# Performance work log

Measured on AMD Instinct MI355X. Metric: run time of the kernel, lower is better.

The kernel has to match this reference:

```python
import jax, jax.numpy as jnp
import numpy as np

BLOCK = 32       # MX block size
EMAX_E4M3 = 8.0  # max exponent of fp8 e4m3 (max normal = 448 = 1.75 * 2^8)
NUM_HEADS = 16


def _e4m3_round(v):
    """Round values to fp8 e4m3 grid (bias 7, 3 mantissa bits, subnormals, max 448)."""
    absv = jnp.abs(v)
    e = jnp.floor(jnp.log2(jnp.where(absv > 0, absv, 1.0)))
    e = jnp.maximum(e, -6.0)                # min normal exponent; below -> subnormal grid
    step = jnp.exp2(e - 3.0)                # 3 mantissa bits
    q = jnp.round(v / step) * step          # round-half-even like IEEE
    q = jnp.clip(q, -448.0, 448.0)
    return jnp.where(absv > 0, q, jnp.zeros_like(q))


def _mx_quantize(x):
    """Blockwise (32 along last dim) shared-exponent (E8M0) fp8 e4m3 quant-dequant."""
    shp = x.shape
    xb = x.reshape(shp[:-1] + (shp[-1] // BLOCK, BLOCK))
    amax = jnp.max(jnp.abs(xb), axis=-1, keepdims=True)
    sexp = jnp.floor(jnp.log2(jnp.where(amax > 0, amax, 1.0))) - EMAX_E4M3
    sexp = jnp.clip(sexp, -127.0, 127.0)    # E8M0 scale range
    scale = jnp.where(amax > 0, jnp.exp2(sexp), jnp.ones_like(sexp))
    q = _e4m3_round(xb / scale) * scale
    return q.reshape(shp)


def mxq(x):
    return _mx_quantize(x)


def _mx_linear(x, W, b):
    # quantize activations and weights (blocks of 32 along the contraction dim)
    return jnp.einsum('bse,oe->bso', mxq(x), mxq(W)) + b


def setup_inputs() -> dict:
    key = jax.random.key(0)
    ks = jax.random.split(key, 9)
    B, S, E = 4, 1024, 1024
    inp = {
        'query': jax.random.normal(ks[0], (B, S, E), dtype=jnp.float32),
        'Wq': jax.random.normal(ks[1], (E, E), dtype=jnp.float32) * 0.02,
        'bq': jnp.zeros((E,), dtype=jnp.float32),
        'Wk': jax.random.normal(ks[2], (E, E), dtype=jnp.float32) * 0.02,
        'bk': jnp.zeros((E,), dtype=jnp.float32),
        'Wv': jax.random.normal(ks[3], (E, E), dtype=jnp.float32) * 0.02,
        'bv': jnp.zeros((E,), dtype=jnp.float32),
        'Wo': jax.random.normal(ks[4], (E, E), dtype=jnp.float32) * 0.02,
        'bo': jnp.zeros((E,), dtype=jnp.float32),
    }
    return inp


def reference(query, Wq, bq, Wk, bk, Wv, bv, Wo, bo):
    B, S, E = query.shape
    H = NUM_HEADS
    D = E // H
    Q = _mx_linear(query, Wq, bq).reshape(B, S, H, D).transpose(0, 2, 1, 3)
    K = _mx_linear(query, Wk, bk).reshape(B, S, H, D).transpose(0, 2, 1, 3)
    V = _mx_linear(query, Wv, bv).reshape(B, S, H, D).transpose(0, 2, 1, 3)
    scores = jnp.einsum('bhqd,bhkd->bhqk', Q, K) / jnp.sqrt(jnp.float32(D))
    scores = mxq(scores)                    # score quantizer (blocks of 32 along kv dim)
    attn = jax.nn.softmax(scores, axis=-1)  # dropout p=0 -> identity
    ctx = jnp.einsum('bhqk,bhkd->bhqd', attn, V)
    ctx = ctx.transpose(0, 2, 1, 3).reshape(B, S, E)
    return _mx_linear(ctx, Wo, bo)
```

## Files before the change

kernel.cpp:

```cpp
#include <hip/hip_runtime.h>
#include <hip/hip_bf16.h>
#include <cstdint>
#include <cstddef>


#define S_LEN 1024
#define E_DIM 1024
#define NH    16
#define DH    64
#define BATCH 4
#define NROWS (BATCH * S_LEN)

typedef short          bf16x8  __attribute__((ext_vector_type(8)));
typedef float          f32x4   __attribute__((ext_vector_type(4)));
typedef unsigned short u16x8   __attribute__((ext_vector_type(8)));
typedef unsigned short u16x4   __attribute__((ext_vector_type(4)));
typedef unsigned int   u32x4   __attribute__((ext_vector_type(4)));


__device__ __forceinline__ void mx_scale_bits(float amax, float& scale, float& inv) {
  int eb = (int)(__float_as_uint(amax) >> 23);
  int sb = eb - 8;
  sb = sb < 1 ? 1 : (sb > 253 ? 253 : sb);
  float sc = __uint_as_float((unsigned)sb << 23);
  float iv = __uint_as_float((unsigned)(254 - sb) << 23);
  bool nz = (amax > 0.0f);
  scale = nz ? sc : 1.0f;
  inv   = nz ? iv : 1.0f;
}

__device__ __forceinline__ void qdq2(float& a, float& b) {
  a = fminf(fmaxf(a, -448.0f), 448.0f);
  b = fminf(fmaxf(b, -448.0f), 448.0f);
  int p = __builtin_amdgcn_cvt_pk_fp8_f32(a, b, 0, false);
  a = __builtin_amdgcn_cvt_f32_fp8(p, 0);
  b = __builtin_amdgcn_cvt_f32_fp8(p, 1);
}

__device__ __forceinline__ unsigned short f32_to_bf16_rne(float f) {
  unsigned u = __float_as_uint(f);
  unsigned r = 0x7FFFu + ((u >> 16) & 1u);
  return (unsigned short)((u + r) >> 16);
}

__device__ __forceinline__ float quad_red_max(float x) {
  auto p = __builtin_amdgcn_permlane16_swap(__float_as_uint(x), __float_as_uint(x), false, false);
  x = fmaxf(__uint_as_float(p[0]), __uint_as_float(p[1]));
  auto q = __builtin_amdgcn_permlane32_swap(__float_as_uint(x), __float_as_uint(x), false, false);
  return fmaxf(__uint_as_float(q[0]), __uint_as_float(q[1]));
}
__device__ __forceinline__ float quad_red_min(float x) {
  auto p = __builtin_amdgcn_permlane16_swap(__float_as_uint(x), __float_as_uint(x), false, false);
  x = fminf(__uint_as_float(p[0]), __uint_as_float(p[1]));
  auto q = __builtin_amdgcn_permlane32_swap(__float_as_uint(x), __float_as_uint(x), false, false);
  return fminf(__uint_as_float(q[0]), __uint_as_float(q[1]));
}
__device__ __forceinline__ float quad_red_sum(float x) {
  auto p = __builtin_amdgcn_permlane16_swap(__float_as_uint(x), __float_as_uint(x), false, false);
  x = __uint_as_float(p[0]) + __uint_as_float(p[1]);
  auto q = __builtin_amdgcn_permlane32_swap(__float_as_uint(x), __float_as_uint(x), false, false);
  return __uint_as_float(q[0]) + __uint_as_float(q[1]);
}


__device__ __forceinline__ void mxq_body(const float* __restrict__ in,
                                         unsigned short* __restrict__ out, int b) {
  const float4* p = (const float4*)(in + (size_t)b * 32);
  float v[32];
#pragma unroll
  for (int g = 0; g < 8; ++g) {
    float4 t = p[g];
    v[g * 4 + 0] = t.x; v[g * 4 + 1] = t.y; v[g * 4 + 2] = t.z; v[g * 4 + 3] = t.w;
  }
  float amax = 0.0f;
#pragma unroll
  for (int i = 0; i < 32; ++i) amax = fmaxf(amax, __builtin_fabsf(v[i]));
  float scale, inv;
  mx_scale_bits(amax, scale, inv);
  u16x8* q = (u16x8*)(out + (size_t)b * 32);
#pragma unroll
  for (int g = 0; g < 4; ++g) {
    u16x8 o;
#pragma unroll
    for (int e = 0; e < 8; e += 2) {
      float a = v[g * 8 + e] * inv, c = v[g * 8 + e + 1] * inv;
      qdq2(a, c);
      o[e]     = (unsigned short)(__float_as_uint(a * scale) >> 16);
      o[e + 1] = (unsigned short)(__float_as_uint(c * scale) >> 16);
    }
    q[g] = o;
  }
}

__global__ __launch_bounds__(256)
void mxq_all(const float* __restrict__ x,
             const float* __restrict__ w0, const float* __restrict__ w1,
             const float* __restrict__ w2, const float* __restrict__ w3,
             unsigned short* __restrict__ ox,
             unsigned short* __restrict__ o0, unsigned short* __restrict__ o1,
             unsigned short* __restrict__ o2, unsigned short* __restrict__ o3) {
  int blk = blockIdx.x;
  const float* in;
  unsigned short* out;
  int base;
  if (blk < 512)      { in = x;  out = ox; base = blk; }
  else if (blk < 640) { in = w0; out = o0; base = blk - 512; }
  else if (blk < 768) { in = w1; out = o1; base = blk - 640; }
  else if (blk < 896) { in = w2; out = o2; base = blk - 768; }
  else                { in = w3; out = o3; base = blk - 896; }
  mxq_body(in, out, base * 256 + threadIdx.x);
}


__global__ __launch_bounds__(256)
void gemm_qkv(const unsigned short* __restrict__ XQ,
              const unsigned short* __restrict__ Wqw, const unsigned short* __restrict__ Wkw,
              const unsigned short* __restrict__ Wvw,
              const float* __restrict__ bq, const float* __restrict__ bk,
              const float* __restrict__ bv,
              unsigned short* __restrict__ Qhi, unsigned short* __restrict__ Qlo,
              unsigned short* __restrict__ Khi, unsigned short* __restrict__ Klo,
              unsigned short* __restrict__ Vthi, unsigned short* __restrict__ Vtlo) {
  const int z = blockIdx.z;
  const unsigned short* Bw = (z == 0) ? Wqw : (z == 1) ? Wkw : Wvw;
  const float* bias = (z == 0) ? bq : (z == 1) ? bk : bv;
  unsigned short* Phi = (z == 0) ? Qhi : (z == 1) ? Khi : Vthi;
  unsigned short* Plo = (z == 0) ? Qlo : (z == 1) ? Klo : Vtlo;
  const float pre = (z == 0) ? 0.125f : 1.0f;

  __shared__ unsigned short sA[128 * 64];
  __shared__ unsigned short sB[128 * 64];
  const int tid = threadIdx.x;
  const int w = tid >> 6, ln = tid & 63;
  const int bm = blockIdx.y * 128, bn = blockIdx.x * 128;
  const int wm = (w >> 1) * 64, wn = (w & 1) * 64;
  const int quad = ln >> 4, col = ln & 15;

  f32x4 acc[4][4];
  f32x4 zero = {0.0f, 0.0f, 0.0f, 0.0f};
#pragma unroll
  for (int i = 0; i < 4; ++i)
#pragma unroll
    for (int j = 0; j < 4; ++j) acc[i][j] = zero;

  const int srow = ln >> 3;
  const int gsw  = (ln & 7) ^ srow;
  const int xo0 = (quad ^ (ln & 7)) * 8;
  const int xo1 = ((quad ^ 4) ^ (ln & 7)) * 8;

  for (int k0 = 0; k0 < 1024; k0 += 64) {
    __syncthreads();
#pragma unroll
    for (int q = 0; q < 4; ++q) {
      int row = w * 32 + q * 8 + srow;
      const unsigned short* ga = XQ + (size_t)(bm + row) * 1024 + k0 + gsw * 8;
      const unsigned short* gb = Bw + (size_t)(bn + row) * 1024 + k0 + gsw * 8;
      __builtin_amdgcn_global_load_lds(
          (const __attribute__((address_space(1))) unsigned int*)ga,
          (__attribute__((address_space(3))) unsigned int*)(sA + (w * 32 + q * 8) * 64),
          16, 0, 0);
      __builtin_amdgcn_global_load_lds(
          (const __attribute__((address_space(1))) unsigned int*)gb,
          (__attribute__((address_space(3))) unsigned int*)(sB + (w * 32 + q * 8) * 64),
          16, 0, 0);
    }
    __syncthreads();

#pragma unroll
    for (int ks = 0; ks < 2; ++ks) {
      const int xo = ks ? xo1 : xo0;
      bf16x8 af[4], bf[4];
#pragma unroll
      for (int t = 0; t < 4; ++t) {
        af[t] = *(const bf16x8*)(sA + (wm + t * 16 + col) * 64 + xo);
        bf[t] = *(const bf16x8*)(sB + (wn + t * 16 + col) * 64 + xo);
      }
#pragma unroll
      for (int ti = 0; ti < 4; ++ti)
#pragma unroll
        for (int tj = 0; tj < 4; ++tj)
          acc[ti][tj] = __builtin_amdgcn_mfma_f32_16x16x32_bf16(af[ti], bf[tj], acc[ti][tj], 0, 0, 0);
    }
  }

#pragma unroll
  for (int ti = 0; ti < 4; ++ti) {
#pragma unroll
    for (int tj = 0; tj < 4; ++tj) {
      int n = bn + wn + tj * 16 + col;
      float bv_ = bias[n];
      if (z != 2) {
#pragma unroll
        for (int i = 0; i < 4; ++i) {
          int m = bm + wm + ti * 16 + quad * 4 + i;
          float v = (acc[ti][tj][i] + bv_) * pre;
          unsigned short h = f32_to_bf16_rne(v);
          float hf = __uint_as_float((unsigned)h << 16);
          Phi[(size_t)m * 1024 + n] = h;
          Plo[(size_t)m * 1024 + n] = f32_to_bf16_rne(v - hf);
        }
      } else {
        int m0 = bm + wm + ti * 16 + quad * 4;
        u16x4 h4, l4;
#pragma unroll
        for (int i = 0; i < 4; ++i) {
          float v = acc[ti][tj][i] + bv_;
          unsigned short h = f32_to_bf16_rne(v);
          float hf = __uint_as_float((unsigned)h << 16);
          h4[i] = h;
          l4[i] = f32_to_bf16_rne(v - hf);
        }
        size_t idx = ((size_t)((m0 >> 10) * 1024 + n)) * 1024 + (m0 & 1023);
        *(u16x4*)(Phi + idx) = h4;
        *(u16x4*)(Plo + idx) = l4;
      }
    }
  }
}


__global__ __launch_bounds__(256)
void gemm_o(const unsigned short* __restrict__ A, const unsigned short* __restrict__ Bw,
            const float* __restrict__ bias, float* __restrict__ C) {
  __shared__ unsigned short sA[64 * 64];
  __shared__ unsigned short sB[128 * 64];
  const int tid = threadIdx.x;
  const int w = tid >> 6, ln = tid & 63;
  const int bm = blockIdx.y * 64, bn = blockIdx.x * 128;
  const int wr = (w >> 1) * 32, wc = (w & 1) * 64;
  const int quad = ln >> 4, col = ln & 15;

  f32x4 acc[2][4];
  f32x4 zero = {0.0f, 0.0f, 0.0f, 0.0f};
#pragma unroll
  for (int i = 0; i < 2; ++i)
#pragma unroll
    for (int j = 0; j < 4; ++j) acc[i][j] = zero;

  const int srow = ln >> 3;
  const int gsw  = (ln & 7) ^ srow;
  const int xo0 = (quad ^ (ln & 7)) * 8;
  const int xo1 = ((quad ^ 4) ^ (ln & 7)) * 8;

  for (int k0 = 0; k0 < 1024; k0 += 64) {
    __syncthreads();
#pragma unroll
    for (int qa = 0; qa < 2; ++qa) {
      int row = w * 16 + qa * 8 + srow;
      __builtin_amdgcn_global_load_lds(
          (const __attribute__((address_space(1))) unsigned int*)(A + (size_t)(bm + row) * 1024 + k0 + gsw * 8),
          (__attribute__((address_space(3))) unsigned int*)(sA + (w * 16 + qa * 8) * 64),
          16, 0, 0);
    }
#pragma unroll
    for (int qb = 0; qb < 4; ++qb) {
      int row = w * 32 + qb * 8 + srow;
      __builtin_amdgcn_global_load_lds(
          (const __attribute__((address_space(1))) unsigned int*)(Bw + (size_t)(bn + row) * 1024 + k0 + gsw * 8),
          (__attribute__((address_space(3))) unsigned int*)(sB + (w * 32 + qb * 8) * 64),
          16, 0, 0);
    }
    __syncthreads();

#pragma unroll
    for (int ks = 0; ks < 2; ++ks) {
      const int xo = ks ? xo1 : xo0;
      bf16x8 af[2], bf[4];
#pragma unroll
      for (int t = 0; t < 2; ++t)
        af[t] = *(const bf16x8*)(sA + (wr + t * 16 + col) * 64 + xo);
#pragma unroll
      for (int t = 0; t < 4; ++t)
        bf[t] = *(const bf16x8*)(sB + (wc + t * 16 + col) * 64 + xo);
#pragma unroll
      for (int ti = 0; ti < 2; ++ti)
#pragma unroll
        for (int tj = 0; tj < 4; ++tj)
          acc[ti][tj] = __builtin_amdgcn_mfma_f32_16x16x32_bf16(af[ti], bf[tj], acc[ti][tj], 0, 0, 0);
    }
  }

#pragma unroll
  for (int ti = 0; ti < 2; ++ti) {
#pragma unroll
    for (int tj = 0; tj < 4; ++tj) {
      int n = bn + wc + tj * 16 + col;
      float bv_ = bias[n];
#pragma unroll
      for (int i = 0; i < 4; ++i) {
        int m = bm + wr + ti * 16 + quad * 4 + i;
        C[(size_t)m * 1024 + n] = acc[ti][tj][i] + bv_;
      }
    }
  }
}


__global__ __launch_bounds__(256, 4)
void attn_kernel(const unsigned short* __restrict__ Qhi, const unsigned short* __restrict__ Qlo,
                 const unsigned short* __restrict__ Khi, const unsigned short* __restrict__ Klo,
                 const unsigned short* __restrict__ Vthi, const unsigned short* __restrict__ Vtlo,
                 unsigned short* __restrict__ ctxq) {
  const int tid = threadIdx.x;
  const int id = blockIdx.y * 16 + blockIdx.x;
  const int qt = (id >> 3) & 15;
  const int bh = ((id >> 7) << 3) | (id & 7);
  const int b = bh >> 4, h = bh & 15;
  const int w = tid >> 6, ln = tid & 63, quad = ln >> 4, col = ln & 15;

  __shared__ __align__(16) short sK[16384];

  bf16x8 qh[2], ql[2];
  {
    const size_t qoff = (size_t)(b * 1024 + qt * 64 + w * 16 + col) * 1024 + h * 64 + quad * 8;
    qh[0] = *(const bf16x8*)(Qhi + qoff);
    qh[1] = *(const bf16x8*)(Qhi + qoff + 32);
    ql[0] = *(const bf16x8*)(Qlo + qoff);
    ql[1] = *(const bf16x8*)(Qlo + qoff + 32);
  }

  const unsigned short* gplane = (w == 0) ? Khi : (w == 1) ? Klo : (w == 2) ? Vthi : Vtlo;
  short* splane = sK + w * 4096;
  const int r8 = ln >> 3;
  const int ch = (ln & 7) ^ r8;
  const unsigned short* bp = (w < 2)
      ? gplane + (size_t)(b * 1024 + r8) * 1024 + h * 64 + ch * 8
      : gplane + (size_t)(b * 1024 + h * 64 + r8) * 1024 + ch * 8;
  const int ktstep = (w < 2) ? 65536 : 64;

  const int xo0 = (quad ^ (col & 7)) * 8;
  const int xo1 = ((quad + 4) ^ (col & 7)) * 8;

  f32x4 o[4];
  f32x4 zero = {0.0f, 0.0f, 0.0f, 0.0f};
#pragma unroll
  for (int t = 0; t < 4; ++t) o[t] = zero;
  float m_ = -3.0e38f, l_ = 0.0f;

  const float LOG2E = 1.44269504088896340736f;

#pragma unroll 1
  for (int kt = 0; kt < 16; ++kt) {
    __syncthreads();
#pragma unroll
    for (int g = 0; g < 8; ++g) {
      __builtin_amdgcn_global_load_lds(
          (const __attribute__((address_space(1))) unsigned int*)(bp + g * 8192),
          (__attribute__((address_space(3))) unsigned int*)(splane + g * 512),
          16, 0, 0);
    }
    bp += ktstep;
    __syncthreads();

    f32x4 s[4];
#pragma unroll
    for (int t = 0; t < 4; ++t) s[t] = zero;
#pragma unroll
    for (int t = 0; t < 4; ++t) {
      const int rb = (t * 16 + col) * 64;
#pragma unroll
      for (int ks = 0; ks < 2; ++ks) {
        const int xo = ks ? xo1 : xo0;
        bf16x8 kh = *(const bf16x8*)(sK +        rb + xo);
        bf16x8 kl = *(const bf16x8*)(sK + 4096 + rb + xo);
        s[t] = __builtin_amdgcn_mfma_f32_16x16x32_bf16(kh, ql[ks], s[t], 0, 0, 0);
        s[t] = __builtin_amdgcn_mfma_f32_16x16x32_bf16(kl, qh[ks], s[t], 0, 0, 0);
        s[t] = __builtin_amdgcn_mfma_f32_16x16x32_bf16(kh, qh[ks], s[t], 0, 0, 0);
      }
    }

    float mx0 = fmaxf(fmaxf(fmaxf(s[0][0], s[0][1]), fmaxf(s[0][2], s[0][3])),
                      fmaxf(fmaxf(s[1][0], s[1][1]), fmaxf(s[1][2], s[1][3])));
    float mn0 = fminf(fminf(fminf(s[0][0], s[0][1]), fminf(s[0][2], s[0][3])),
                      fminf(fminf(s[1][0], s[1][1]), fminf(s[1][2], s[1][3])));
    float mx1 = fmaxf(fmaxf(fmaxf(s[2][0], s[2][1]), fmaxf(s[2][2], s[2][3])),
                      fmaxf(fmaxf(s[3][0], s[3][1]), fmaxf(s[3][2], s[3][3])));
    float mn1 = fminf(fminf(fminf(s[2][0], s[2][1]), fminf(s[2][2], s[2][3])),
                      fminf(fminf(s[3][0], s[3][1]), fminf(s[3][2], s[3][3])));
    mx0 = quad_red_max(mx0); mn0 = quad_red_min(mn0);
    mx1 = quad_red_max(mx1); mn1 = quad_red_min(mn1);

    float sc0, iv0, sc1, iv1;
    mx_scale_bits(fmaxf(mx0, -mn0), sc0, iv0);
    mx_scale_bits(fmaxf(mx1, -mn1), sc1, iv1);
    float scl0 = sc0 * LOG2E, scl1 = sc1 * LOG2E;
#pragma unroll
    for (int t = 0; t < 4; ++t) {
      float iv  = (t < 2) ? iv0 : iv1;
      float scl = (t < 2) ? scl0 : scl1;
      float q0 = s[t][0] * iv, q1 = s[t][1] * iv;
      qdq2(q0, q1);
      float q2 = s[t][2] * iv, q3 = s[t][3] * iv;
      qdq2(q2, q3);
      s[t][0] = q0 * scl; s[t][1] = q1 * scl;
      s[t][2] = q2 * scl; s[t][3] = q3 * scl;
    }
    float d0 = mx0 * iv0, d1 = mx1 * iv1;
    qdq2(d0, d1);
    float mt = fmaxf(d0 * scl0, d1 * scl1);

    float mnew  = fmaxf(m_, mt);
    float alpha = __builtin_amdgcn_exp2f(m_ - mnew);
    m_ = mnew;
    l_ *= alpha;
#pragma unroll
    for (int t = 0; t < 4; ++t) {
      float p0 = __builtin_amdgcn_exp2f(s[t][0] - mnew);
      float p1 = __builtin_amdgcn_exp2f(s[t][1] - mnew);
      float p2 = __builtin_amdgcn_exp2f(s[t][2] - mnew);
      float p3 = __builtin_amdgcn_exp2f(s[t][3] - mnew);
      s[t][0] = p0; s[t][1] = p1; s[t][2] = p2; s[t][3] = p3;
      l_ += (p0 + p1) + (p2 + p3);
    }
#pragma unroll
    for (int nt = 0; nt < 4; ++nt)
#pragma unroll
      for (int i = 0; i < 4; ++i) o[nt][i] *= alpha;

    unsigned Wh[4][2], Wl[4][2];
#pragma unroll
    for (int t = 0; t < 4; ++t) {
#pragma unroll
      for (int u = 0; u < 2; ++u) {
        float a = s[t][2 * u], c = s[t][2 * u + 1];
        __hip_bfloat162 h2 = __float22bfloat162_rn(make_float2(a, c));
        unsigned uh = *(unsigned*)&h2;
        float af = __uint_as_float(uh << 16);
        float cf = __uint_as_float(uh & 0xffff0000u);
        __hip_bfloat162 l2 = __float22bfloat162_rn(make_float2(a - af, c - cf));
        Wh[t][u] = uh;
        Wl[t][u] = *(unsigned*)&l2;
      }
    }
    bf16x8 pah[2], pal[2];
#pragma unroll
    for (int ks = 0; ks < 2; ++ks) {
      auto a0  = __builtin_amdgcn_permlane32_swap(Wh[2 * ks][0], Wh[2 * ks + 1][0], false, false);
      auto j02 = __builtin_amdgcn_permlane16_swap(a0[0], a0[1], false, false);
      auto a1  = __builtin_amdgcn_permlane32_swap(Wh[2 * ks][1], Wh[2 * ks + 1][1], false, false);
      auto j13 = __builtin_amdgcn_permlane16_swap(a1[0], a1[1], false, false);
      u32x4 hw; hw[0] = j02[0]; hw[1] = j13[0]; hw[2] = j02[1]; hw[3] = j13[1];
      pah[ks] = __builtin_bit_cast(bf16x8, hw);
      auto b0  = __builtin_amdgcn_permlane32_swap(Wl[2 * ks][0], Wl[2 * ks + 1][0], false, false);
      auto k02 = __builtin_amdgcn_permlane16_swap(b0[0], b0[1], false, false);
      auto b1  = __builtin_amdgcn_permlane32_swap(Wl[2 * ks][1], Wl[2 * ks + 1][1], false, false);
      auto k13 = __builtin_amdgcn_permlane16_swap(b1[0], b1[1], false, false);
      u32x4 lw; lw[0] = k02[0]; lw[1] = k13[0]; lw[2] = k02[1]; lw[3] = k13[1];
      pal[ks] = __builtin_bit_cast(bf16x8, lw);
    }

#pragma unroll
    for (int nt = 0; nt < 4; ++nt) {
      const int rb = (nt * 16 + col) * 64;
#pragma unroll
      for (int ks = 0; ks < 2; ++ks) {
        const int xo = ks ? xo1 : xo0;
        bf16x8 vh = *(const bf16x8*)(sK +  8192 + rb + xo);
        bf16x8 vl = *(const bf16x8*)(sK + 12288 + rb + xo);
        o[nt] = __builtin_amdgcn_mfma_f32_16x16x32_bf16(vh, pal[ks], o[nt], 0, 0, 0);
        o[nt] = __builtin_amdgcn_mfma_f32_16x16x32_bf16(vl, pah[ks], o[nt], 0, 0, 0);
        o[nt] = __builtin_amdgcn_mfma_f32_16x16x32_bf16(vh, pah[ks], o[nt], 0, 0, 0);
      }
    }
  }

  float linv = 1.0f / quad_red_sum(l_);
#pragma unroll
  for (int nt = 0; nt < 4; ++nt)
#pragma unroll
    for (int i = 0; i < 4; ++i) o[nt][i] *= linv;

  float am0 = 0.0f, am1 = 0.0f;
#pragma unroll
  for (int i = 0; i < 4; ++i) {
    am0 = fmaxf(am0, fmaxf(__builtin_fabsf(o[0][i]), __builtin_fabsf(o[1][i])));
    am1 = fmaxf(am1, fmaxf(__builtin_fabsf(o[2][i]), __builtin_fabsf(o[3][i])));
  }
  am0 = quad_red_max(am0);
  am1 = quad_red_max(am1);
  float sc0, iv0, sc1, iv1;
  mx_scale_bits(am0, sc0, iv0);
  mx_scale_bits(am1, sc1, iv1);

  const int tok = b * 1024 + qt * 64 + w * 16 + col;
  const size_t base = (size_t)tok * 1024 + h * 64 + quad * 4;
#pragma unroll
  for (int nt = 0; nt < 4; ++nt) {
    float iv = (nt < 2) ? iv0 : iv1;
    float sc = (nt < 2) ? sc0 : sc1;
    float q0 = o[nt][0] * iv, q1 = o[nt][1] * iv;
    qdq2(q0, q1);
    float q2 = o[nt][2] * iv, q3 = o[nt][3] * iv;
    qdq2(q2, q3);
    u16x4 h4;
    h4[0] = (unsigned short)(__float_as_uint(q0 * sc) >> 16);
    h4[1] = (unsigned short)(__float_as_uint(q1 * sc) >> 16);
    h4[2] = (unsigned short)(__float_as_uint(q2 * sc) >> 16);
    h4[3] = (unsigned short)(__float_as_uint(q3 * sc) >> 16);
    *(u16x4*)(ctxq + base + nt * 16) = h4;
  }
}


extern "C" void kernel_launch(void* const* d_in, const int* in_sizes, int n_in,
                              void* d_out, int out_size, void* d_ws, size_t ws_size,
                              hipStream_t stream) {
  (void)in_sizes; (void)n_in; (void)out_size; (void)ws_size;
  const float* x  = (const float*)d_in[0];
  const float* Wq = (const float*)d_in[1];
  const float* bq = (const float*)d_in[2];
  const float* Wk = (const float*)d_in[3];
  const float* bk = (const float*)d_in[4];
  const float* Wv = (const float*)d_in[5];
  const float* bv = (const float*)d_in[6];
  const float* Wo = (const float*)d_in[7];
  const float* bo = (const float*)d_in[8];

  char* wsb = (char*)d_ws;
  const size_t MB = (size_t)1 << 20;
  unsigned short* XQb   = (unsigned short*)(wsb + 0);
  unsigned short* WQb   = (unsigned short*)(wsb + 8 * MB);
  unsigned short* WKb   = (unsigned short*)(wsb + 10 * MB);
  unsigned short* WVb   = (unsigned short*)(wsb + 12 * MB);
  unsigned short* WOb   = (unsigned short*)(wsb + 14 * MB);
  unsigned short* Qhi   = (unsigned short*)(wsb + 16 * MB);
  unsigned short* Qlo   = (unsigned short*)(wsb + 24 * MB);
  unsigned short* Khi   = (unsigned short*)(wsb + 32 * MB);
  unsigned short* Klo   = (unsigned short*)(wsb + 40 * MB);
  unsigned short* Vthi  = (unsigned short*)(wsb + 48 * MB);
  unsigned short* Vtlo  = (unsigned short*)(wsb + 56 * MB);
  unsigned short* CTXQb = XQb;

  mxq_all<<<1024, 256, 0, stream>>>(x, Wq, Wk, Wv, Wo, XQb, WQb, WKb, WVb, WOb);

  dim3 qkvgrid(E_DIM / 128, NROWS / 128, 3);
  gemm_qkv<<<qkvgrid, 256, 0, stream>>>(XQb, WQb, WKb, WVb, bq, bk, bv,
                                        Qhi, Qlo, Khi, Klo, Vthi, Vtlo);

  dim3 agrid(16, 64);
  attn_kernel<<<agrid, 256, 0, stream>>>(Qhi, Qlo, Khi, Klo, Vthi, Vtlo, CTXQb);

  dim3 ogrid(E_DIM / 128, NROWS / 64);
  gemm_o<<<ogrid, 256, 0, stream>>>(CTXQb, WOb, bo, (float*)d_out);
}
```

Measured before the change: 234.6 us.

## Double-buffer projection GEMMs, remap blocks per XCD, and skip softmax rescaling

Both projection GEMMs now use double-buffered LDS: the next K tile is prefetched with global_load_lds while the current one feeds the MFMAs, with explicit vmcnt waits and barriers replacing the two syncthreads per iteration. Block indices are remapped so consecutive blocks on the same XCD share M rows, which is meant to improve L2 reuse. The attention kernel now skips the online-softmax max update and the rescaling of the accumulator unless some lane's tile max exceeds the running max by more than 4 (log2 units). The extra LDS halves the number of resident blocks, and the lazy rescale lets exponentials reach up to 2^4 before renormalising.

```diff
diff --git a/kernel.cpp b/kernel.cpp
--- a/kernel.cpp
+++ b/kernel.cpp
@@ -128,11 +128,13 @@
   unsigned short* Plo = (z == 0) ? Qlo : (z == 1) ? Klo : Vtlo;
   const float pre = (z == 0) ? 0.125f : 1.0f;
 
-  __shared__ unsigned short sA[128 * 64];
-  __shared__ unsigned short sB[128 * 64];
+  __shared__ unsigned short sA[2][128 * 64];
+  __shared__ unsigned short sB[2][128 * 64];
   const int tid = threadIdx.x;
   const int w = tid >> 6, ln = tid & 63;
-  const int bm = blockIdx.y * 128, bn = blockIdx.x * 128;
+  const int fid = blockIdx.y * 8 + blockIdx.x;
+  const int xcd = fid & 7, sq = fid >> 3;
+  const int bm = (xcd * 4 + (sq & 3)) * 128, bn = (sq >> 2) * 128;
   const int wm = (w >> 1) * 64, wn = (w & 1) * 64;
   const int quad = ln >> 4, col = ln & 15;
 
@@ -148,8 +150,7 @@
   const int xo0 = (quad ^ (ln & 7)) * 8;
   const int xo1 = ((quad ^ 4) ^ (ln & 7)) * 8;
 
-  for (int k0 = 0; k0 < 1024; k0 += 64) {
-    __syncthreads();
+  auto STAGE = [&](int bb, int k0) {
 #pragma unroll
     for (int q = 0; q < 4; ++q) {
       int row = w * 32 + q * 8 + srow;
@@ -157,30 +158,47 @@
       const unsigned short* gb = Bw + (size_t)(bn + row) * 1024 + k0 + gsw * 8;
       __builtin_amdgcn_global_load_lds(
           (const __attribute__((address_space(1))) unsigned int*)ga,
-          (__attribute__((address_space(3))) unsigned int*)(sA + (w * 32 + q * 8) * 64),
+          (__attribute__((address_space(3))) unsigned int*)(&sA[bb][0] + (w * 32 + q * 8) * 64),
           16, 0, 0);
       __builtin_amdgcn_global_load_lds(
           (const __attribute__((address_space(1))) unsigned int*)gb,
-          (__attribute__((address_space(3))) unsigned int*)(sB + (w * 32 + q * 8) * 64),
+          (__attribute__((address_space(3))) unsigned int*)(&sB[bb][0] + (w * 32 + q * 8) * 64),
           16, 0, 0);
     }
-    __syncthreads();
-
+  };
+
+  STAGE(0, 0);
+#pragma unroll 1
+  for (int k0 = 0; k0 < 1024; k0 += 64) {
+    const int cur = (k0 >> 6) & 1;
+    if (k0 < 960) {
+      STAGE(cur ^ 1, k0 + 64);
+      asm volatile("s_waitcnt vmcnt(8)" ::: "memory");
+    } else {
+      asm volatile("s_waitcnt vmcnt(0)" ::: "memory");
+    }
+    __builtin_amdgcn_s_barrier();
+    __builtin_amdgcn_sched_barrier(0);
+
+    const unsigned short* pA = &sA[cur][0];
+    const unsigned short* pB = &sB[cur][0];
 #pragma unroll
     for (int ks = 0; ks < 2; ++ks) {
       const int xo = ks ? xo1 : xo0;
-      bf16x8 af[4], bf[4];
+      bf16x8 af[4], bfr[4];
 #pragma unroll
       for (int t = 0; t < 4; ++t) {
-        af[t] = *(const bf16x8*)(sA + (wm + t * 16 + col) * 64 + xo);
-        bf[t] = *(const bf16x8*)(sB + (wn + t * 16 + col) * 64 + xo);
+        af[t]  = *(const bf16x8*)(pA + (wm + t * 16 + col) * 64 + xo);
+        bfr[t] = *(const bf16x8*)(pB + (wn + t * 16 + col) * 64 + xo);
       }
 #pragma unroll
       for (int ti = 0; ti < 4; ++ti)
 #pragma unroll
         for (int tj = 0; tj < 4; ++tj)
-          acc[ti][tj] = __builtin_amdgcn_mfma_f32_16x16x32_bf16(af[ti], bf[tj], acc[ti][tj], 0, 0, 0);
-    }
+          acc[ti][tj] = __builtin_amdgcn_mfma_f32_16x16x32_bf16(af[ti], bfr[tj], acc[ti][tj], 0, 0, 0);
+    }
+    __builtin_amdgcn_sched_barrier(0);
+    __builtin_amdgcn_s_barrier();
   }
 
 #pragma unroll
@@ -222,11 +240,13 @@
 __global__ __launch_bounds__(256)
 void gemm_o(const unsigned short* __restrict__ A, const unsigned short* __restrict__ Bw,
             const float* __restrict__ bias, float* __restrict__ C) {
-  __shared__ unsigned short sA[64 * 64];
-  __shared__ unsigned short sB[128 * 64];
+  __shared__ unsigned short sA[2][64 * 64];
+  __shared__ unsigned short sB[2][128 * 64];
   const int tid = threadIdx.x;
   const int w = tid >> 6, ln = tid & 63;
-  const int bm = blockIdx.y * 64, bn = blockIdx.x * 128;
+  const int fid = blockIdx.y * 8 + blockIdx.x;
+  const int xcd = fid & 7, sq = fid >> 3;
+  const int bm = (xcd * 8 + (sq & 7)) * 64, bn = (sq >> 3) * 128;
   const int wr = (w >> 1) * 32, wc = (w & 1) * 64;
   const int quad = ln >> 4, col = ln & 15;
 
@@ -242,14 +262,13 @@
   const int xo0 = (quad ^ (ln & 7)) * 8;
   const int xo1 = ((quad ^ 4) ^ (ln & 7)) * 8;
 
-  for (int k0 = 0; k0 < 1024; k0 += 64) {
-    __syncthreads();
+  auto STAGE = [&](int bb, int k0) {
 #pragma unroll
     for (int qa = 0; qa < 2; ++qa) {
       int row = w * 16 + qa * 8 + srow;
       __builtin_amdgcn_global_load_lds(
           (const __attribute__((address_space(1))) unsigned int*)(A + (size_t)(bm + row) * 1024 + k0 + gsw * 8),
-          (__attribute__((address_space(3))) unsigned int*)(sA + (w * 16 + qa * 8) * 64),
+          (__attribute__((address_space(3))) unsigned int*)(&sA[bb][0] + (w * 16 + qa * 8) * 64),
           16, 0, 0);
     }
 #pragma unroll
@@ -257,27 +276,44 @@
       int row = w * 32 + qb * 8 + srow;
       __builtin_amdgcn_global_load_lds(
           (const __attribute__((address_space(1))) unsigned int*)(Bw + (size_t)(bn + row) * 1024 + k0 + gsw * 8),
-          (__attribute__((address_space(3))) unsigned int*)(sB + (w * 32 + qb * 8) * 64),
+          (__attribute__((address_space(3))) unsigned int*)(&sB[bb][0] + (w * 32 + qb * 8) * 64),
           16, 0, 0);
     }
-    __syncthreads();
-
+  };
+
+  STAGE(0, 0);
+#pragma unroll 1
+  for (int k0 = 0; k0 < 1024; k0 += 64) {
+    const int cur = (k0 >> 6) & 1;
+    if (k0 < 960) {
+      STAGE(cur ^ 1, k0 + 64);
+      asm volatile("s_waitcnt vmcnt(6)" ::: "memory");
+    } else {
+      asm volatile("s_waitcnt vmcnt(0)" ::: "memory");
+    }
+    __builtin_amdgcn_s_barrier();
+    __builtin_amdgcn_sched_barrier(0);
+
+    const unsigned short* pA = &sA[cur][0];
+    const unsigned short* pB = &sB[cur][0];
 #pragma unroll
     for (int ks = 0; ks < 2; ++ks) {
       const int xo = ks ? xo1 : xo0;
-      bf16x8 af[2], bf[4];
+      bf16x8 af[2], bfr[4];
 #pragma unroll
       for (int t = 0; t < 2; ++t)
-        af[t] = *(const bf16x8*)(sA + (wr + t * 16 + col) * 64 + xo);
+        af[t] = *(const bf16x8*)(pA + (wr + t * 16 + col) * 64 + xo);
 #pragma unroll
       for (int t = 0; t < 4; ++t)
-        bf[t] = *(const bf16x8*)(sB + (wc + t * 16 + col) * 64 + xo);
+        bfr[t] = *(const bf16x8*)(pB + (wc + t * 16 + col) * 64 + xo);
 #pragma unroll
       for (int ti = 0; ti < 2; ++ti)
 #pragma unroll
         for (int tj = 0; tj < 4; ++tj)
-          acc[ti][tj] = __builtin_amdgcn_mfma_f32_16x16x32_bf16(af[ti], bf[tj], acc[ti][tj], 0, 0, 0);
-    }
+          acc[ti][tj] = __builtin_amdgcn_mfma_f32_16x16x32_bf16(af[ti], bfr[tj], acc[ti][tj], 0, 0, 0);
+    }
+    __builtin_amdgcn_sched_barrier(0);
+    __builtin_amdgcn_s_barrier();
   }
 
 #pragma unroll
@@ -399,23 +435,25 @@
     qdq2(d0, d1);
     float mt = fmaxf(d0 * scl0, d1 * scl1);
 
-    float mnew  = fmaxf(m_, mt);
-    float alpha = __builtin_amdgcn_exp2f(m_ - mnew);
-    m_ = mnew;
-    l_ *= alpha;
+    if (__any(mt > m_ + 4.0f)) {
+      float mnew  = fmaxf(m_, mt);
+      float alpha = __builtin_amdgcn_exp2f(m_ - mnew);
+      m_ = mnew;
+      l_ *= alpha;
+#pragma unroll
+      for (int nt = 0; nt < 4; ++nt)
+#pragma unroll
+        for (int i = 0; i < 4; ++i) o[nt][i] *= alpha;
+    }
 #pragma unroll
     for (int t = 0; t < 4; ++t) {
-      float p0 = __builtin_amdgcn_exp2f(s[t][0] - mnew);
-      float p1 = __builtin_amdgcn_exp2f(s[t][1] - mnew);
-      float p2 = __builtin_amdgcn_exp2f(s[t][2] - mnew);
-      float p3 = __builtin_amdgcn_exp2f(s[t][3] - mnew);
+      float p0 = __builtin_amdgcn_exp2f(s[t][0] - m_);
+      float p1 = __builtin_amdgcn_exp2f(s[t][1] - m_);
+      float p2 = __builtin_amdgcn_exp2f(s[t][2] - m_);
+      float p3 = __builtin_amdgcn_exp2f(s[t][3] - m_);
       s[t][0] = p0; s[t][1] = p1; s[t][2] = p2; s[t][3] = p3;
       l_ += (p0 + p1) + (p2 + p3);
     }
-#pragma unroll
-    for (int nt = 0; nt < 4; ++nt)
-#pragma unroll
-      for (int i = 0; i < 4; ++i) o[nt][i] *= alpha;
 
     unsigned Wh[4][2], Wl[4][2];
 #pragma unroll
```

New measurement: 222.2 us. -5.3%, faster.
